# Kernel tuning notes

Measured on AMD Instinct MI355X. Metric: run time of the kernel, lower is better.

The kernel has to match this reference:

```python
import jax, jax.numpy as jnp
import numpy as np

B, S, E, H = 4, 1024, 1024, 16
HD = E // H  # 64


def setup_inputs() -> dict:
    key = jax.random.key(0)
    ks = jax.random.split(key, 9)
    scale = 1.0 / np.sqrt(E)
    x = jax.random.normal(ks[0], (B, S, E), dtype=jnp.float32)
    attention_mask = jnp.ones((B, S, S), dtype=jnp.int32)
    # per-head projection weights, batched over heads: [H, E, HD]
    Wq = jax.random.normal(ks[1], (H, E, HD), dtype=jnp.float32) * scale
    Wk = jax.random.normal(ks[2], (H, E, HD), dtype=jnp.float32) * scale
    Wv = jax.random.normal(ks[3], (H, E, HD), dtype=jnp.float32) * scale
    bq = jax.random.normal(ks[4], (H, HD), dtype=jnp.float32) * scale
    bk = jax.random.normal(ks[5], (H, HD), dtype=jnp.float32) * scale
    bv = jax.random.normal(ks[6], (H, HD), dtype=jnp.float32) * scale
    # output projection, torch Linear convention: [out_features, in_features]
    Wo = jax.random.normal(ks[7], (E, E), dtype=jnp.float32) * scale
    bo = jax.random.normal(ks[8], (E,), dtype=jnp.float32) * scale
    return {"x": x, "attention_mask": attention_mask, "Wq": Wq, "bq": bq,
            "Wk": Wk, "bk": bk, "Wv": Wv, "bv": bv, "Wo": Wo, "bo": bo}


def reference(x, attention_mask, Wq, bq, Wk, bk, Wv, bv, Wo, bo):
    # batched-over-heads QKV projections: (B,S,E) x (H,E,HD) -> (B,H,S,HD)
    q = jnp.einsum('bse,hed->bhsd', x, Wq) + bq[None, :, None, :]
    k = jnp.einsum('bse,hed->bhsd', x, Wk) + bk[None, :, None, :]
    v = jnp.einsum('bse,hed->bhsd', x, Wv) + bv[None, :, None, :]
    scores = jnp.einsum('bhsd,bhtd->bhst', q, k) / jnp.sqrt(jnp.float32(HD))
    mask = attention_mask[:, None, :, :]  # (B,1,S,S) broadcast over heads
    scores = jnp.where(mask == 0, -jnp.inf, scores)
    weights = jax.nn.softmax(scores, axis=-1)
    out = jnp.einsum('bhst,bhtd->bhsd', weights, v)
    # concat heads on last dim: (B,S,H*HD) == (B,S,E)
    out = out.transpose(0, 2, 1, 3).reshape(B, S, E)
    return out @ Wo.T + bo
```

## Files before the change

kernel.cpp:

```cpp
#include <hip/hip_runtime.h>
#include <hip/hip_bf16.h>

#define NB 4
#define SEQ 1024
#define EMB 1024
#define NH 16
#define HD 64

typedef unsigned short u16;
typedef __attribute__((ext_vector_type(8))) __bf16 bf16x8;
typedef __attribute__((ext_vector_type(8))) short short8;
typedef __attribute__((ext_vector_type(4))) float floatx4;

__device__ inline u16 f2b_rn(float f) {
    union { float f; unsigned int i; } x; x.f = f;
    unsigned int r = (x.i + 0x7FFFu + ((x.i >> 16) & 1u)) >> 16;
    return (u16)r;
}
__device__ inline bf16x8 s2b(short8 v) {
    union { short8 s; bf16x8 b; } x; x.s = v; return x.b;
}

__device__ inline void gload_lds16(const void* g, void* l) {
    __builtin_amdgcn_global_load_lds(
        (const __attribute__((address_space(1))) void*)g,
        (__attribute__((address_space(3))) void*)l, 16, 0, 0);
}

__device__ inline bf16x8 ldsfrag(const u16* base, int r, int c) {
    return s2b(*(const short8*)&base[r * 64 + (c ^ ((r & 7) * 8))]);
}

__device__ inline void cvt8(const float* __restrict__ s, u16* __restrict__ d) {
    float4 a = *(const float4*)(s);
    float4 b = *(const float4*)(s + 4);
    union { u16 u[8]; int4 v; } o;
    o.u[0] = f2b_rn(a.x); o.u[1] = f2b_rn(a.y); o.u[2] = f2b_rn(a.z); o.u[3] = f2b_rn(a.w);
    o.u[4] = f2b_rn(b.x); o.u[5] = f2b_rn(b.y); o.u[6] = f2b_rn(b.z); o.u[7] = f2b_rn(b.w);
    *(int4*)(d) = o.v;
}

__global__ __launch_bounds__(256) void prep(
    const float* __restrict__ x, const float* __restrict__ Wq,
    const float* __restrict__ Wk, const float* __restrict__ Wv,
    const int* __restrict__ mask,
    u16* __restrict__ xb, u16* __restrict__ Wt,
    unsigned long long* __restrict__ bits)
{
    __shared__ u16 T[64 * 80];
    int bx = blockIdx.x;
    int tid = threadIdx.x;

    if (bx < 512) {
        #pragma unroll
        for (int c = 0; c < 4; ++c) {
            int i = (bx * 4 + c) * 2048 + tid * 8;
            cvt8(x + i, xb + i);
        }
    } else if (bx < 1280) {
        int bx2 = bx - 512;
        int e0 = (bx2 & 15) * 64;
        int ph = bx2 >> 4;
        int p = ph >> 4, h = ph & 15;
        const float* W = (p == 0 ? Wq : (p == 1 ? Wk : Wv)) + h * (EMB * HD);
        #pragma unroll
        for (int c = 0; c < 2; ++c) {
            int flat = c * 2048 + tid * 8;
            int r = flat >> 6;
            int d = flat & 63;
            cvt8(W + (size_t)(e0 + r) * HD + d, &T[r * 80 + d]);
        }
        __syncthreads();
        int d = tid >> 2;
        int ec = tid & 3;
        union { u16 u[16]; int4 v[2]; } tmp;
        #pragma unroll
        for (int i = 0; i < 16; ++i) tmp.u[i] = T[(ec * 16 + i) * 80 + d];
        u16* dst = Wt + ((size_t)(p * NH + h) * HD + d) * EMB + e0 + ec * 16;
        *(int4*)(dst) = tmp.v[0];
        *(int4*)(dst + 8) = tmp.v[1];
    } else {
        int base = (bx - 1280) * 16 + (tid >> 6) * 4;
        int lane = tid & 63;
        #pragma unroll
        for (int i = 0; i < 4; ++i) {
            int gw = base + i;
            int m = mask[(size_t)gw * 64 + lane];
            unsigned long long bl = __ballot(m != 0);
            if (lane == 0) bits[gw] = bl;
        }
    }
}

#define BARX do { __builtin_amdgcn_sched_barrier(0); __builtin_amdgcn_s_barrier(); __builtin_amdgcn_sched_barrier(0); } while(0)
#define VMCNT6 asm volatile("s_waitcnt vmcnt(6)" ::: "memory")
#define VMCNT2 asm volatile("s_waitcnt vmcnt(2)" ::: "memory")
#define VMCNT0 asm volatile("s_waitcnt vmcnt(0)" ::: "memory")

__device__ __forceinline__ void rd_b(const u16* B, int wn, int ln, int quad, bf16x8 (&bfr)[4][2]) {
    #pragma unroll
    for (int nc = 0; nc < 4; ++nc) {
        bfr[nc][0] = ldsfrag(B, wn * 64 + nc * 16 + ln, quad * 8);
        bfr[nc][1] = ldsfrag(B, wn * 64 + nc * 16 + ln, 32 + quad * 8);
    }
}
__device__ __forceinline__ void rd_a(const u16* A, int wm, int mf0, int ln, int quad, bf16x8 (&a)[2][2]) {
    #pragma unroll
    for (int jj = 0; jj < 2; ++jj) {
        a[jj][0] = ldsfrag(A, wm * 128 + (mf0 + jj) * 16 + ln, quad * 8);
        a[jj][1] = ldsfrag(A, wm * 128 + (mf0 + jj) * 16 + ln, 32 + quad * 8);
    }
}
__device__ __forceinline__ void mm8(floatx4 (&acc)[8][4], const bf16x8 (&a)[2][2],
                                    const bf16x8 (&bfr)[4][2], int mf0) {
    #pragma unroll
    for (int jj = 0; jj < 2; ++jj)
        #pragma unroll
        for (int nc = 0; nc < 4; ++nc) {
            acc[mf0 + jj][nc] = __builtin_amdgcn_mfma_f32_16x16x32_bf16(a[jj][0], bfr[nc][0], acc[mf0 + jj][nc], 0, 0, 0);
            acc[mf0 + jj][nc] = __builtin_amdgcn_mfma_f32_16x16x32_bf16(a[jj][1], bfr[nc][1], acc[mf0 + jj][nc], 0, 0, 0);
        }
}

#define STG(srcb, buf, c, kt) gload_lds16((srcb) + (size_t)(c) * 65536 + (kt) * 64 + soff, (buf) + (c) * 4096 + ldst)

__global__ __launch_bounds__(512, 2) void qkv_gemm(
    const u16* __restrict__ x,
    const u16* __restrict__ Wt2,
    const float* __restrict__ bq, const float* __restrict__ bk, const float* __restrict__ bv,
    u16* __restrict__ Q, u16* __restrict__ K, u16* __restrict__ Vt)
{
    __shared__ u16 L[65536];
    u16* A0s = L;
    u16* A1s = L + 16384;
    u16* B0s = L + 32768;
    u16* B1s = L + 49152;

    int gid = blockIdx.x;
    int xcd = gid & 7;
    int j   = gid >> 3;
    int mt_ = (xcd >> 1) * 4 + (j & 3);
    int nt_ = (xcd & 1) * 6 + (j >> 2);
    int m0 = mt_ * 256;
    int n0 = nt_ * 256;

    int tid = threadIdx.x;
    int w = tid >> 6, lane = tid & 63, quad = lane >> 4, ln = lane & 15;
    int wm = w >> 2, wn = w & 3;

    const u16* Asrc = x   + (size_t)m0 * EMB;
    const u16* Bsrc = Wt2 + (size_t)n0 * EMB;

    int sr = tid >> 3;
    int sc = ((tid & 7) ^ (sr & 7)) * 8;
    size_t soff = (size_t)sr * EMB + sc;
    int ldst = w * 512;

    STG(Asrc, A0s, 0, 0); STG(Asrc, A0s, 1, 0); STG(Asrc, A0s, 2, 0); STG(Asrc, A0s, 3, 0);
    STG(Bsrc, B0s, 0, 0); STG(Bsrc, B0s, 1, 0); STG(Bsrc, B0s, 2, 0); STG(Bsrc, B0s, 3, 0);
    STG(Bsrc, B1s, 0, 1); STG(Bsrc, B1s, 1, 1); STG(Bsrc, B1s, 2, 1); STG(Bsrc, B1s, 3, 1);
    STG(Asrc, A1s, 0, 1); STG(Asrc, A1s, 2, 1);
    VMCNT6;
    BARX;

    floatx4 acc[8][4] = {};
    bf16x8 bfr[4][2];
    bf16x8 a[2][2];

    for (int i = 0; i < 8; ++i) {
        const int T = 2 * i;
        const bool st = (i < 7);
        rd_b(B0s, wn, ln, quad, bfr);
        rd_a(A0s, wm, 0, ln, quad, a);
        STG(Asrc, A1s, 1, T + 1); STG(Asrc, A1s, 3, T + 1);
        BARX;
        __builtin_amdgcn_s_setprio(1); mm8(acc, a, bfr, 0); __builtin_amdgcn_s_setprio(0);
        BARX;
        rd_a(A0s, wm, 2, ln, quad, a);
        if (st) { STG(Bsrc, B0s, 0, T + 2); STG(Bsrc, B0s, 1, T + 2); }
        BARX;
        __builtin_amdgcn_s_setprio(1); mm8(acc, a, bfr, 2); __builtin_amdgcn_s_setprio(0);
        BARX;
        rd_a(A0s, wm, 4, ln, quad, a);
        if (st) { STG(Bsrc, B0s, 2, T + 2); STG(Bsrc, B0s, 3, T + 2); }
        BARX;
        __builtin_amdgcn_s_setprio(1); mm8(acc, a, bfr, 4); __builtin_amdgcn_s_setprio(0);
        BARX;
        rd_a(A0s, wm, 6, ln, quad, a);
        if (st) { STG(Asrc, A0s, 0, T + 2); STG(Asrc, A0s, 2, T + 2); }
        BARX;
        __builtin_amdgcn_s_setprio(1); mm8(acc, a, bfr, 6); __builtin_amdgcn_s_setprio(0);
        if (st) { VMCNT6; } else { VMCNT0; }
        BARX;
        rd_b(B1s, wn, ln, quad, bfr);
        rd_a(A1s, wm, 0, ln, quad, a);
        if (st) { STG(Asrc, A0s, 1, T + 2); STG(Asrc, A0s, 3, T + 2); }
        BARX;
        __builtin_amdgcn_s_setprio(1); mm8(acc, a, bfr, 0); __builtin_amdgcn_s_setprio(0);
        BARX;
        rd_a(A1s, wm, 2, ln, quad, a);
        if (st) { STG(Bsrc, B1s, 0, T + 3); STG(Bsrc, B1s, 1, T + 3); }
        BARX;
        __builtin_amdgcn_s_setprio(1); mm8(acc, a, bfr, 2); __builtin_amdgcn_s_setprio(0);
        BARX;
        rd_a(A1s, wm, 4, ln, quad, a);
        if (st) { STG(Bsrc, B1s, 2, T + 3); STG(Bsrc, B1s, 3, T + 3); }
        BARX;
        __builtin_amdgcn_s_setprio(1); mm8(acc, a, bfr, 4); __builtin_amdgcn_s_setprio(0);
        BARX;
        rd_a(A1s, wm, 6, ln, quad, a);
        if (st) { STG(Asrc, A1s, 0, T + 3); STG(Asrc, A1s, 2, T + 3); }
        BARX;
        __builtin_amdgcn_s_setprio(1); mm8(acc, a, bfr, 6); __builtin_amdgcn_s_setprio(0);
        if (st) { VMCNT6; }
        BARX;
    }

    int nbase = n0 + wn * 64;
    int p = nbase >> 10;
    int h = (nbase >> 6) & 15;
    const float* bias = (p == 0 ? bq : (p == 1 ? bk : bv));
    if (p < 2) {
        u16* Out = (p == 0) ? Q : K;
        float qs = (p == 0) ? 0.125f * 1.44269504f : 1.0f;
        #pragma unroll
        for (int nc = 0; nc < 4; ++nc) {
            int d = nc * 16 + ln;
            float bv_ = bias[(nbase & 1023) + d];
            #pragma unroll
            for (int mf = 0; mf < 8; ++mf) {
                #pragma unroll
                for (int reg = 0; reg < 4; ++reg) {
                    int m = m0 + wm * 128 + mf * 16 + quad * 4 + reg;
                    int b_ = m >> 10, s = m & 1023;
                    Out[((size_t)(b_ * NH + h) * SEQ + s) * HD + d] = f2b_rn((acc[mf][nc][reg] + bv_) * qs);
                }
            }
        }
    } else {
        #pragma unroll
        for (int nc = 0; nc < 4; ++nc) {
            int d = nc * 16 + ln;
            float bv_ = bias[(nbase & 1023) + d];
            #pragma unroll
            for (int mf = 0; mf < 8; ++mf) {
                int m = m0 + wm * 128 + mf * 16 + quad * 4;
                int b_ = m >> 10, s = m & 1023;
                union { u16 u[4]; uint2 v; } pk;
                #pragma unroll
                for (int reg = 0; reg < 4; ++reg)
                    pk.u[reg] = f2b_rn(acc[mf][nc][reg] + bv_);
                *(uint2*)&Vt[((size_t)(b_ * NH + h) * HD + d) * SEQ + s] = pk.v;
            }
        }
    }
}

__device__ __forceinline__ void astage(const u16* __restrict__ Kb, const u16* __restrict__ Vb,
                                       u16* Kd, u16* Vd, int t0, int tid) {
    #pragma unroll
    for (int i = 0; i < 2; ++i) {
        int flat0 = i * 256 + (tid & 192);
        int flat = flat0 + (tid & 63);
        int r = flat >> 3;
        int c = ((flat & 7) ^ (r & 7)) * 8;
        gload_lds16(Kb + (size_t)(t0 + r) * HD + c, Kd + flat0 * 8);
        gload_lds16(Vb + (size_t)r * SEQ + t0 + c, Vd + flat0 * 8);
    }
}

__device__ __forceinline__ void attn_tile(
    const u16* Ksc, const u16* Vsc, u16* Ps,
    const bf16x8 (&qf)[2][2], floatx4 (&o)[2][5],
    unsigned long long bm0, unsigned long long bm1,
    int w, int ln, int quad)
{
    const int PP = 72;
    floatx4 sc[2][4] = {};
    #pragma unroll
    for (int kk = 0; kk < 2; ++kk) {
        bf16x8 kf[4];
        #pragma unroll
        for (int tb = 0; tb < 4; ++tb)
            kf[tb] = ldsfrag(Ksc, tb * 16 + ln, kk * 32 + quad * 8);
        __builtin_amdgcn_s_setprio(1);
        #pragma unroll
        for (int s = 0; s < 2; ++s)
            #pragma unroll
            for (int tb = 0; tb < 4; ++tb)
                sc[s][tb] = __builtin_amdgcn_mfma_f32_16x16x32_bf16(kf[tb], qf[s][kk], sc[s][tb], 0, 0, 0);
        __builtin_amdgcn_s_setprio(0);
    }

    #pragma unroll
    for (int s = 0; s < 2; ++s) {
        unsigned long long bm = s ? bm1 : bm0;
        if (__any(bm != ~0ull)) {
            #pragma unroll
            for (int tb = 0; tb < 4; ++tb)
                #pragma unroll
                for (int reg = 0; reg < 4; ++reg)
                    if (!((bm >> (tb * 16 + quad * 4 + reg)) & 1)) sc[s][tb][reg] = -1e30f;
        }
    }

    #pragma unroll
    for (int s = 0; s < 2; ++s) {
        int mrow = w * 32 + s * 16 + ln;
        #pragma unroll
        for (int tb = 0; tb < 4; ++tb) {
            union { float f; unsigned int i; } e0_, e1_, e2_, e3_;
            e0_.f = __builtin_amdgcn_exp2f(sc[s][tb][0]);
            e1_.f = __builtin_amdgcn_exp2f(sc[s][tb][1]);
            e2_.f = __builtin_amdgcn_exp2f(sc[s][tb][2]);
            e3_.f = __builtin_amdgcn_exp2f(sc[s][tb][3]);
            uint2 pk;
            pk.x = ((e0_.i + 0x8000u) >> 16) | ((e1_.i + 0x8000u) & 0xFFFF0000u);
            pk.y = ((e2_.i + 0x8000u) >> 16) | ((e3_.i + 0x8000u) & 0xFFFF0000u);
            *(uint2*)&Ps[mrow * PP + tb * 16 + quad * 4] = pk;
        }
    }

    #pragma unroll
    for (int kk = 0; kk < 2; ++kk) {
        bf16x8 vf[5];
        #pragma unroll
        for (int dt = 0; dt < 5; ++dt)
            vf[dt] = ldsfrag(Vsc, dt * 16 + ln, kk * 32 + quad * 8);
        #pragma unroll
        for (int s = 0; s < 2; ++s) {
            bf16x8 pf = s2b(*(const short8*)&Ps[(w * 32 + s * 16 + ln) * PP + kk * 32 + quad * 8]);
            __builtin_amdgcn_s_setprio(1);
            #pragma unroll
            for (int dt = 0; dt < 5; ++dt)
                o[s][dt] = __builtin_amdgcn_mfma_f32_16x16x32_bf16(pf, vf[dt], o[s][dt], 0, 0, 0);
            __builtin_amdgcn_s_setprio(0);
        }
    }
}

__global__ __launch_bounds__(256) void attn(
    const u16* __restrict__ Q, const u16* __restrict__ K, const u16* __restrict__ Vt,
    const unsigned long long* __restrict__ bits,
    const float* __restrict__ Wo, u16* __restrict__ Wob,
    u16* __restrict__ Aout)
{
    __shared__ u16 L[16512 + 128 * 72];
    u16* Ks0 = L;
    u16* Ks1 = L + 4096;
    u16* Vs0 = L + 8192;
    u16* Vs1 = L + 12352;
    u16* Ps  = L + 16512;

    int bid = blockIdx.x;
    int tid = threadIdx.x;

    if (bid >= 512) {
        int i = (bid - 512) * 2048 + tid * 8;
        cvt8(Wo + i, Wob + i);
        return;
    }

    int bh = bid & 63;
    int q0 = (bid >> 6) * 128;
    int b = bh >> 4, h = bh & 15;
    const u16* Qb = Q  + (size_t)bh * SEQ * HD;
    const u16* Kb = K  + (size_t)bh * SEQ * HD;
    const u16* Vb = Vt + (size_t)bh * HD * SEQ;

    int w = tid >> 6, lane = tid & 63, quad = lane >> 4, ln = lane & 15;

    if (tid < 32) {
        u16* dst = (tid < 16 ? L + 12288 : L + 16448) + (tid & 15) * 4;
        *(uint2*)dst = make_uint2(0x3F803F80u, 0x3F803F80u);
    }

    bf16x8 qf[2][2];
    #pragma unroll
    for (int s = 0; s < 2; ++s) {
        const u16* qp = Qb + (size_t)(q0 + w * 32 + s * 16 + ln) * HD + quad * 8;
        union { int4 i; bf16x8 b; } c0, c1;
        c0.i = *(const int4*)(qp);
        c1.i = *(const int4*)(qp + 32);
        qf[s][0] = c0.b; qf[s][1] = c1.b;
    }

    __syncthreads();

    astage(Kb, Vb, Ks0, Vs0, 0,  tid);
    astage(Kb, Vb, Ks1, Vs1, 64, tid);
    size_t bb0 = ((size_t)b * SEQ + q0 + w * 32 + ln) * 16;
    size_t bb1 = bb0 + 256;
    unsigned long long bmn0 = bits[bb0];
    unsigned long long bmn1 = bits[bb1];

    floatx4 o[2][5] = {};

    for (int i = 0; i < 8; ++i) {
        VMCNT6;
        BARX;
        {
            unsigned long long bc0 = bmn0, bc1 = bmn1;
            bmn0 = bits[bb0 + (2 * i + 1)];
            bmn1 = bits[bb1 + (2 * i + 1)];
            attn_tile(Ks0, Vs0, Ps, qf, o, bc0, bc1, w, ln, quad);
        }
        BARX;
        if (i < 7) astage(Kb, Vb, Ks0, Vs0, i * 128 + 128, tid);
        if (i < 7) { VMCNT6; } else { VMCNT2; }
        BARX;
        {
            unsigned long long bc0 = bmn0, bc1 = bmn1;
            if (i < 7) { bmn0 = bits[bb0 + (2 * i + 2)]; bmn1 = bits[bb1 + (2 * i + 2)]; }
            attn_tile(Ks1, Vs1, Ps, qf, o, bc0, bc1, w, ln, quad);
        }
        BARX;
        if (i < 7) astage(Kb, Vb, Ks1, Vs1, i * 128 + 192, tid);
    }

    #pragma unroll
    for (int s = 0; s < 2; ++s) {
        #pragma unroll
        for (int reg = 0; reg < 4; ++reg) {
            float l = __shfl(o[s][4][reg], lane & 48, 64);
            float inv = 1.0f / l;
            int m = q0 + w * 32 + s * 16 + quad * 4 + reg;
            #pragma unroll
            for (int dt = 0; dt < 4; ++dt)
                Aout[((size_t)b * SEQ + m) * EMB + h * HD + dt * 16 + ln] = f2b_rn(o[s][dt][reg] * inv);
        }
    }
}

__global__ __launch_bounds__(256) void out_proj(
    const u16* __restrict__ A,
    const u16* __restrict__ Wo,
    const float* __restrict__ bo,
    float* __restrict__ Out)
{
    __shared__ u16 As[64 * 64];
    __shared__ u16 Bs[128 * 64];

    int gid = blockIdx.x;
    int xcd = gid & 7;
    int j   = gid >> 3;
    int m0 = (xcd * 8 + (j & 7)) * 64;
    int n0 = (j >> 3) * 128;

    int tid = threadIdx.x;
    int w = tid >> 6, lane = tid & 63, quad = lane >> 4, ln = lane & 15;
    int wm = w & 1, wn = w >> 1;

    floatx4 acc[2][4] = {};

    for (int k0 = 0; k0 < EMB; k0 += 64) {
        __syncthreads();
        #pragma unroll
        for (int i = 0; i < 2; ++i) {
            int flat0 = i * 256 + (tid & 192);
            int flat = flat0 + lane;
            int r = flat >> 3;
            int c = ((flat & 7) ^ (r & 7)) * 8;
            gload_lds16(A + (size_t)(m0 + r) * EMB + k0 + c, As + flat0 * 8);
        }
        #pragma unroll
        for (int i = 0; i < 4; ++i) {
            int flat0 = i * 256 + (tid & 192);
            int flat = flat0 + lane;
            int r = flat >> 3;
            int c = ((flat & 7) ^ (r & 7)) * 8;
            gload_lds16(Wo + (size_t)(n0 + r) * EMB + k0 + c, Bs + flat0 * 8);
        }
        __syncthreads();

        #pragma unroll
        for (int kk = 0; kk < 2; ++kk) {
            bf16x8 a[2], bfr[4];
            #pragma unroll
            for (int mt = 0; mt < 2; ++mt)
                a[mt] = ldsfrag(As, wm * 32 + mt * 16 + ln, kk * 32 + quad * 8);
            #pragma unroll
            for (int nc = 0; nc < 4; ++nc)
                bfr[nc] = ldsfrag(Bs, wn * 64 + nc * 16 + ln, kk * 32 + quad * 8);
            #pragma unroll
            for (int mt = 0; mt < 2; ++mt)
                #pragma unroll
                for (int nc = 0; nc < 4; ++nc)
                    acc[mt][nc] = __builtin_amdgcn_mfma_f32_16x16x32_bf16(a[mt], bfr[nc], acc[mt][nc], 0, 0, 0);
        }
    }

    #pragma unroll
    for (int nc = 0; nc < 4; ++nc) {
        int n = n0 + wn * 64 + nc * 16 + ln;
        float bb = bo[n];
        #pragma unroll
        for (int mt = 0; mt < 2; ++mt) {
            #pragma unroll
            for (int reg = 0; reg < 4; ++reg) {
                int m = m0 + wm * 32 + mt * 16 + quad * 4 + reg;
                Out[(size_t)m * EMB + n] = acc[mt][nc][reg] + bb;
            }
        }
    }
}

extern "C" void kernel_launch(void* const* d_in, const int* in_sizes, int n_in,
                              void* d_out, int out_size, void* d_ws, size_t ws_size,
                              hipStream_t stream) {
    const float* x  = (const float*)d_in[0];
    const int*   mk = (const int*)d_in[1];
    const float* Wq = (const float*)d_in[2];
    const float* bq = (const float*)d_in[3];
    const float* Wk = (const float*)d_in[4];
    const float* bk = (const float*)d_in[5];
    const float* Wv = (const float*)d_in[6];
    const float* bv = (const float*)d_in[7];
    const float* Wo = (const float*)d_in[8];
    const float* bo = (const float*)d_in[9];
    float* out = (float*)d_out;

    const size_t MB = 1u << 20;
    char* ws = (char*)d_ws;
    u16* xb  = (u16*)ws;
    u16* Wt  = (u16*)(ws + 8 * MB);
    u16* Wob = (u16*)(ws + 14 * MB);
    unsigned long long* bits = (unsigned long long*)(ws + 16 * MB);
    u16* Qw  = (u16*)(ws + 16 * MB + 512 * 1024);
    u16* Kw  = (u16*)(ws + 24 * MB + 512 * 1024);
    u16* Vtw = (u16*)(ws + 32 * MB + 512 * 1024);
    u16* Ao  = xb;

    prep<<<5376, 256, 0, stream>>>(x, Wq, Wk, Wv, mk, xb, Wt, bits);
    qkv_gemm<<<192, 512, 0, stream>>>(xb, Wt, bq, bk, bv, Qw, Kw, Vtw);
    attn<<<1024, 256, 0, stream>>>(Qw, Kw, Vtw, bits, Wo, Wob, Ao);
    out_proj<<<512, 256, 0, stream>>>(Ao, Wob, bo, out);
}
```

Before: 184.7 us.

## Move mask/Wo prep into QKV GEMM idle blocks and double-buffer out_proj

Mask bit-packing and the Wo bf16 conversion move out of prep and attn into 64 extra blocks of the QKV GEMM launch, so they run alongside the 192 GEMM tiles and use CUs that would otherwise sit idle. The attn launch shrinks to its real 512 blocks. out_proj is rewritten to use 512-thread blocks with 64x256 tiles and double-buffered async global-to-LDS loads paced by vmcnt waits. In exchange, the mask loop runs 128 serial iterations per wave and could become a straggler inside the GEMM launch, and the larger out_proj tiles give fewer blocks (256).

```diff
diff --git a/kernel.cpp b/kernel.cpp
--- a/kernel.cpp
+++ b/kernel.cpp
@@ -40,12 +40,16 @@
     *(int4*)(d) = o.v;
 }
 
+#define BARX do { __builtin_amdgcn_sched_barrier(0); __builtin_amdgcn_s_barrier(); __builtin_amdgcn_sched_barrier(0); } while(0)
+#define VMCNT6 asm volatile("s_waitcnt vmcnt(6)" ::: "memory")
+#define VMCNT5 asm volatile("s_waitcnt vmcnt(5)" ::: "memory")
+#define VMCNT2 asm volatile("s_waitcnt vmcnt(2)" ::: "memory")
+#define VMCNT0 asm volatile("s_waitcnt vmcnt(0)" ::: "memory")
+
 __global__ __launch_bounds__(256) void prep(
     const float* __restrict__ x, const float* __restrict__ Wq,
     const float* __restrict__ Wk, const float* __restrict__ Wv,
-    const int* __restrict__ mask,
-    u16* __restrict__ xb, u16* __restrict__ Wt,
-    unsigned long long* __restrict__ bits)
+    u16* __restrict__ xb, u16* __restrict__ Wt)
 {
     __shared__ u16 T[64 * 80];
     int bx = blockIdx.x;
@@ -57,7 +61,7 @@
             int i = (bx * 4 + c) * 2048 + tid * 8;
             cvt8(x + i, xb + i);
         }
-    } else if (bx < 1280) {
+    } else {
         int bx2 = bx - 512;
         int e0 = (bx2 & 15) * 64;
         int ph = bx2 >> 4;
@@ -79,23 +83,8 @@
         u16* dst = Wt + ((size_t)(p * NH + h) * HD + d) * EMB + e0 + ec * 16;
         *(int4*)(dst) = tmp.v[0];
         *(int4*)(dst + 8) = tmp.v[1];
-    } else {
-        int base = (bx - 1280) * 16 + (tid >> 6) * 4;
-        int lane = tid & 63;
-        #pragma unroll
-        for (int i = 0; i < 4; ++i) {
-            int gw = base + i;
-            int m = mask[(size_t)gw * 64 + lane];
-            unsigned long long bl = __ballot(m != 0);
-            if (lane == 0) bits[gw] = bl;
-        }
-    }
-}
-
-#define BARX do { __builtin_amdgcn_sched_barrier(0); __builtin_amdgcn_s_barrier(); __builtin_amdgcn_sched_barrier(0); } while(0)
-#define VMCNT6 asm volatile("s_waitcnt vmcnt(6)" ::: "memory")
-#define VMCNT2 asm volatile("s_waitcnt vmcnt(2)" ::: "memory")
-#define VMCNT0 asm volatile("s_waitcnt vmcnt(0)" ::: "memory")
+    }
+}
 
 __device__ __forceinline__ void rd_b(const u16* B, int wn, int ln, int quad, bf16x8 (&bfr)[4][2]) {
     #pragma unroll
@@ -128,7 +117,9 @@
     const u16* __restrict__ x,
     const u16* __restrict__ Wt2,
     const float* __restrict__ bq, const float* __restrict__ bk, const float* __restrict__ bv,
-    u16* __restrict__ Q, u16* __restrict__ K, u16* __restrict__ Vt)
+    const int* __restrict__ mask, const float* __restrict__ Wo,
+    u16* __restrict__ Q, u16* __restrict__ K, u16* __restrict__ Vt,
+    u16* __restrict__ Wob, unsigned long long* __restrict__ bits)
 {
     __shared__ u16 L[65536];
     u16* A0s = L;
@@ -137,6 +128,27 @@
     u16* B1s = L + 49152;
 
     int gid = blockIdx.x;
+    int tid = threadIdx.x;
+
+    if (gid >= 192) {
+        int sb = gid - 192;
+        #pragma unroll
+        for (int c2 = 0; c2 < 4; ++c2) {
+            int i = (sb * 4 + c2) * 4096 + tid * 8;
+            cvt8(Wo + i, Wob + i);
+        }
+        int lane = tid & 63;
+        int r0 = sb * 1024 + (tid >> 6) * 128;
+        #pragma unroll 4
+        for (int i = 0; i < 128; ++i) {
+            int gw = r0 + i;
+            int m = mask[(size_t)gw * 64 + lane];
+            unsigned long long bl = __ballot(m != 0);
+            if (lane == 0) bits[gw] = bl;
+        }
+        return;
+    }
+
     int xcd = gid & 7;
     int j   = gid >> 3;
     int mt_ = (xcd >> 1) * 4 + (j & 3);
@@ -144,7 +156,6 @@
     int m0 = mt_ * 256;
     int n0 = nt_ * 256;
 
-    int tid = threadIdx.x;
     int w = tid >> 6, lane = tid & 63, quad = lane >> 4, ln = lane & 15;
     int wm = w >> 2, wn = w & 3;
 
@@ -342,7 +353,6 @@
 __global__ __launch_bounds__(256) void attn(
     const u16* __restrict__ Q, const u16* __restrict__ K, const u16* __restrict__ Vt,
     const unsigned long long* __restrict__ bits,
-    const float* __restrict__ Wo, u16* __restrict__ Wob,
     u16* __restrict__ Aout)
 {
     __shared__ u16 L[16512 + 128 * 72];
@@ -355,12 +365,6 @@
     int bid = blockIdx.x;
     int tid = threadIdx.x;
 
-    if (bid >= 512) {
-        int i = (bid - 512) * 2048 + tid * 8;
-        cvt8(Wo + i, Wob + i);
-        return;
-    }
-
     int bh = bid & 63;
     int q0 = (bid >> 6) * 128;
     int b = bh >> 4, h = bh & 15;
@@ -432,74 +436,93 @@
     }
 }
 
-__global__ __launch_bounds__(256) void out_proj(
+#define OSTG_A(buf, kt) gload_lds16(Asrc + (size_t)(kt) * 64 + soff, (buf) + ldst)
+#define OSTG_B(buf, c, kt) gload_lds16(Bsrc + (size_t)(c) * 65536 + (size_t)(kt) * 64 + soff, (buf) + (c) * 4096 + ldst)
+
+__device__ __forceinline__ void op_tile(const u16* As, const u16* Bs,
+                                        floatx4 (&acc)[4][2], int w, int ln, int quad)
+{
+    #pragma unroll
+    for (int kk = 0; kk < 2; ++kk) {
+        bf16x8 av[4], bv2[2];
+        #pragma unroll
+        for (int mf = 0; mf < 4; ++mf)
+            av[mf] = ldsfrag(As, mf * 16 + ln, kk * 32 + quad * 8);
+        #pragma unroll
+        for (int nc = 0; nc < 2; ++nc)
+            bv2[nc] = ldsfrag(Bs, w * 32 + nc * 16 + ln, kk * 32 + quad * 8);
+        __builtin_amdgcn_s_setprio(1);
+        #pragma unroll
+        for (int mf = 0; mf < 4; ++mf)
+            #pragma unroll
+            for (int nc = 0; nc < 2; ++nc)
+                acc[mf][nc] = __builtin_amdgcn_mfma_f32_16x16x32_bf16(av[mf], bv2[nc], acc[mf][nc], 0, 0, 0);
+        __builtin_amdgcn_s_setprio(0);
+    }
+}
+
+__global__ __launch_bounds__(512, 2) void out_proj(
     const u16* __restrict__ A,
     const u16* __restrict__ Wo,
     const float* __restrict__ bo,
     float* __restrict__ Out)
 {
-    __shared__ u16 As[64 * 64];
-    __shared__ u16 Bs[128 * 64];
+    __shared__ u16 L[40960];
+    u16* A0s = L;
+    u16* A1s = L + 4096;
+    u16* B0s = L + 8192;
+    u16* B1s = L + 24576;
 
     int gid = blockIdx.x;
     int xcd = gid & 7;
     int j   = gid >> 3;
     int m0 = (xcd * 8 + (j & 7)) * 64;
-    int n0 = (j >> 3) * 128;
+    int n0 = (j >> 3) * 256;
 
     int tid = threadIdx.x;
     int w = tid >> 6, lane = tid & 63, quad = lane >> 4, ln = lane & 15;
-    int wm = w & 1, wn = w >> 1;
-
-    floatx4 acc[2][4] = {};
-
-    for (int k0 = 0; k0 < EMB; k0 += 64) {
-        __syncthreads();
-        #pragma unroll
-        for (int i = 0; i < 2; ++i) {
-            int flat0 = i * 256 + (tid & 192);
-            int flat = flat0 + lane;
-            int r = flat >> 3;
-            int c = ((flat & 7) ^ (r & 7)) * 8;
-            gload_lds16(A + (size_t)(m0 + r) * EMB + k0 + c, As + flat0 * 8);
-        }
-        #pragma unroll
-        for (int i = 0; i < 4; ++i) {
-            int flat0 = i * 256 + (tid & 192);
-            int flat = flat0 + lane;
-            int r = flat >> 3;
-            int c = ((flat & 7) ^ (r & 7)) * 8;
-            gload_lds16(Wo + (size_t)(n0 + r) * EMB + k0 + c, Bs + flat0 * 8);
-        }
-        __syncthreads();
-
-        #pragma unroll
-        for (int kk = 0; kk < 2; ++kk) {
-            bf16x8 a[2], bfr[4];
-            #pragma unroll
-            for (int mt = 0; mt < 2; ++mt)
-                a[mt] = ldsfrag(As, wm * 32 + mt * 16 + ln, kk * 32 + quad * 8);
-            #pragma unroll
-            for (int nc = 0; nc < 4; ++nc)
-                bfr[nc] = ldsfrag(Bs, wn * 64 + nc * 16 + ln, kk * 32 + quad * 8);
-            #pragma unroll
-            for (int mt = 0; mt < 2; ++mt)
-                #pragma unroll
-                for (int nc = 0; nc < 4; ++nc)
-                    acc[mt][nc] = __builtin_amdgcn_mfma_f32_16x16x32_bf16(a[mt], bfr[nc], acc[mt][nc], 0, 0, 0);
-        }
-    }
-
-    #pragma unroll
-    for (int nc = 0; nc < 4; ++nc) {
-        int n = n0 + wn * 64 + nc * 16 + ln;
+
+    const u16* Asrc = A  + (size_t)m0 * EMB;
+    const u16* Bsrc = Wo + (size_t)n0 * EMB;
+    int sr = tid >> 3;
+    int sc = ((tid & 7) ^ (sr & 7)) * 8;
+    size_t soff = (size_t)sr * EMB + sc;
+    int ldst = w * 512;
+
+    OSTG_A(A0s, 0); OSTG_B(B0s, 0, 0); OSTG_B(B0s, 1, 0); OSTG_B(B0s, 2, 0); OSTG_B(B0s, 3, 0);
+    OSTG_A(A1s, 1); OSTG_B(B1s, 0, 1); OSTG_B(B1s, 1, 1); OSTG_B(B1s, 2, 1); OSTG_B(B1s, 3, 1);
+
+    floatx4 acc[4][2] = {};
+
+    for (int i = 0; i < 8; ++i) {
+        VMCNT5;
+        BARX;
+        op_tile(A0s, B0s, acc, w, ln, quad);
+        BARX;
+        if (i < 7) {
+            int kt = 2 * i + 2;
+            OSTG_A(A0s, kt); OSTG_B(B0s, 0, kt); OSTG_B(B0s, 1, kt); OSTG_B(B0s, 2, kt); OSTG_B(B0s, 3, kt);
+        }
+        if (i < 7) { VMCNT5; } else { VMCNT0; }
+        BARX;
+        op_tile(A1s, B1s, acc, w, ln, quad);
+        BARX;
+        if (i < 7) {
+            int kt = 2 * i + 3;
+            OSTG_A(A1s, kt); OSTG_B(B1s, 0, kt); OSTG_B(B1s, 1, kt); OSTG_B(B1s, 2, kt); OSTG_B(B1s, 3, kt);
+        }
+    }
+
+    #pragma unroll
+    for (int nc = 0; nc < 2; ++nc) {
+        int n = n0 + w * 32 + nc * 16 + ln;
         float bb = bo[n];
         #pragma unroll
-        for (int mt = 0; mt < 2; ++mt) {
+        for (int mf = 0; mf < 4; ++mf) {
             #pragma unroll
             for (int reg = 0; reg < 4; ++reg) {
-                int m = m0 + wm * 32 + mt * 16 + quad * 4 + reg;
-                Out[(size_t)m * EMB + n] = acc[mt][nc][reg] + bb;
+                int m = m0 + mf * 16 + quad * 4 + reg;
+                Out[(size_t)m * EMB + n] = acc[mf][nc][reg] + bb;
             }
         }
     }
@@ -531,8 +554,8 @@
     u16* Vtw = (u16*)(ws + 32 * MB + 512 * 1024);
     u16* Ao  = xb;
 
-    prep<<<5376, 256, 0, stream>>>(x, Wq, Wk, Wv, mk, xb, Wt, bits);
-    qkv_gemm<<<192, 512, 0, stream>>>(xb, Wt, bq, bk, bv, Qw, Kw, Vtw);
-    attn<<<1024, 256, 0, stream>>>(Qw, Kw, Vtw, bits, Wo, Wob, Ao);
-    out_proj<<<512, 256, 0, stream>>>(Ao, Wob, bo, out);
-}
+    prep<<<1280, 256, 0, stream>>>(x, Wq, Wk, Wv, xb, Wt);
+    qkv_gemm<<<256, 512, 0, stream>>>(xb, Wt, bq, bk, bv, mk, Wo, Qw, Kw, Vtw, Wob, bits);
+    attn<<<512, 256, 0, stream>>>(Qw, Kw, Vtw, bits, Ao);
+    out_proj<<<256, 512, 0, stream>>>(Ao, Wob, bo, out);
+}
```

After: 212.9 us. +15.3%, slower.
